# Performance work log

Hardware: AMD Instinct MI355X
Metric: run time of the kernel (lower is better)

The kernel has to match this reference:

```python
import jax, jax.numpy as jnp
import numpy as np

B, S, HID = 1, 2048, 2048
NUM_HEADS, NUM_KV_HEADS, HEAD_DIM = 16, 4, 128
ROPE_THETA = 10000.0
EPS = 1e-6


def setup_inputs() -> dict:
    key = jax.random.key(0)
    ks = jax.random.split(key, 9)
    s = 0.02
    return {
        "hidden_states": jax.random.normal(ks[0], (B, S, HID), jnp.float32),
        "mu_prev": jax.random.normal(ks[1], (B, S, HID), jnp.float32),
        "wq": jax.random.normal(ks[2], (NUM_HEADS * HEAD_DIM, HID), jnp.float32) * s,
        "wk": jax.random.normal(ks[3], (NUM_KV_HEADS * HEAD_DIM, HID), jnp.float32) * s,
        "wv": jax.random.normal(ks[4], (NUM_KV_HEADS * HEAD_DIM, HID), jnp.float32) * s,
        "wo": jax.random.normal(ks[5], (HID, NUM_HEADS * HEAD_DIM), jnp.float32) * s,
        "wmq": jax.random.normal(ks[6], (NUM_HEADS * HEAD_DIM, HID), jnp.float32) * (s * 0.1),
        "wmk": jax.random.normal(ks[7], (NUM_KV_HEADS * HEAD_DIM, HID), jnp.float32) * (s * 0.1),
        "wmv": jax.random.normal(ks[8], (NUM_KV_HEADS * HEAD_DIM, HID), jnp.float32) * (s * 0.1),
        "q_norm_w": jnp.ones((HEAD_DIM,), jnp.float32),
        "k_norm_w": jnp.ones((HEAD_DIM,), jnp.float32),
    }


def _rmsnorm(x, w):
    var = jnp.mean(jnp.square(x), axis=-1, keepdims=True)
    return x * jax.lax.rsqrt(var + EPS) * w


def _rope_cos_sin(seq_len, dtype):
    inv_freq = 1.0 / (ROPE_THETA ** (jnp.arange(0, HEAD_DIM, 2, dtype=jnp.float32) / HEAD_DIM))
    freqs = jnp.arange(seq_len, dtype=jnp.float32)[:, None] * inv_freq[None, :]  # [S, D/2]
    emb = jnp.concatenate([freqs, freqs], axis=-1)  # [S, D]
    return jnp.cos(emb).astype(dtype), jnp.sin(emb).astype(dtype)


def _rotate_half(x):
    x1, x2 = jnp.split(x, 2, axis=-1)
    return jnp.concatenate([-x2, x1], axis=-1)


def reference(hidden_states, mu_prev, wq, wk, wv, wo, wmq, wmk, wmv, q_norm_w, k_norm_w):
    b, s, _ = hidden_states.shape
    # Fused mu-guided QKV projections (cat(x, mu) @ cat(W, Wm)^T == x@W^T + mu@Wm^T)
    q = hidden_states @ wq.T + mu_prev @ wmq.T  # [B,S,H*D]
    k = hidden_states @ wk.T + mu_prev @ wmk.T  # [B,S,KV*D]
    v = hidden_states @ wv.T + mu_prev @ wmv.T
    q = q.reshape(b, s, NUM_HEADS, HEAD_DIM).transpose(0, 2, 1, 3)      # [B,H,S,D]
    k = k.reshape(b, s, NUM_KV_HEADS, HEAD_DIM).transpose(0, 2, 1, 3)   # [B,KV,S,D]
    v = v.reshape(b, s, NUM_KV_HEADS, HEAD_DIM).transpose(0, 2, 1, 3)
    # per-head QK RMSNorm
    q = _rmsnorm(q, q_norm_w)
    k = _rmsnorm(k, k_norm_w)
    # RoPE
    cos, sin = _rope_cos_sin(s, q.dtype)
    q = q * cos + _rotate_half(q) * sin
    k = k * cos + _rotate_half(k) * sin
    # GQA attention without materializing repeated K/V: group query heads
    g = NUM_HEADS // NUM_KV_HEADS
    qg = q.reshape(b, NUM_KV_HEADS, g, s, HEAD_DIM)
    scale = 1.0 / jnp.sqrt(jnp.asarray(HEAD_DIM, q.dtype))
    scores = jnp.einsum('bkgqd,bkld->bkgql', qg, k) * scale  # [B,KV,G,S,S]
    causal = jnp.tril(jnp.ones((s, s), bool))
    scores = jnp.where(causal, scores, jnp.asarray(-jnp.inf, scores.dtype))
    probs = jax.nn.softmax(scores.astype(jnp.float32), axis=-1).astype(q.dtype)
    out = jnp.einsum('bkgql,bkld->bkgqd', probs, v)  # [B,KV,G,S,D]
    out = out.reshape(b, NUM_HEADS, s, HEAD_DIM).transpose(0, 2, 1, 3).reshape(b, s, NUM_HEADS * HEAD_DIM)
    return out @ wo.T
```

## Files before the change

kernel.cpp:

```cpp
#include <hip/hip_runtime.h>
#include <math.h>

#define SEQ 2048
#define HID_DIM 2048
#define NH 16
#define NKV 4
#define HD 128
#define QS 3072

typedef float  f4v  __attribute__((ext_vector_type(4)));
typedef __bf16 bf8v __attribute__((ext_vector_type(8)));
typedef __bf16 bf4v __attribute__((ext_vector_type(4)));
typedef __bf16 bf2v __attribute__((ext_vector_type(2)));

typedef __attribute__((address_space(1))) const void* gvp;
typedef __attribute__((address_space(3))) void*       svp;

__device__ __forceinline__ void gld16(const void* g, void* lds_wave_base) {
    __builtin_amdgcn_global_load_lds((gvp)g, (svp)lds_wave_base, 16, 0, 0);
}

__global__ __launch_bounds__(256)
void cvt_cat2(__bf16* __restrict__ dst, const float* __restrict__ s0,
              const float* __restrict__ s1, int rows, int kq)
{
    int i = blockIdx.x * 256 + threadIdx.x;
    if (i >= rows * kq * 2) return;
    int row = i / (2 * kq), c = i - row * 2 * kq;
    const float* s = (c < kq) ? s0 + ((size_t)row * kq + c) * 4
                              : s1 + ((size_t)row * kq + (c - kq)) * 4;
    float4 v = *reinterpret_cast<const float4*>(s);
    *reinterpret_cast<bf4v*>(dst + ((size_t)row * 2 * kq + c) * 4) =
        bf4v{ (__bf16)v.x, (__bf16)v.y, (__bf16)v.z, (__bf16)v.w };
}

__global__ __launch_bounds__(256)
void cvt(__bf16* __restrict__ dst, const float* __restrict__ src, int n4)
{
    int i = blockIdx.x * 256 + threadIdx.x;
    if (i >= n4) return;
    float4 v = *reinterpret_cast<const float4*>(src + (size_t)i * 4);
    *reinterpret_cast<bf4v*>(dst + (size_t)i * 4) =
        bf4v{ (__bf16)v.x, (__bf16)v.y, (__bf16)v.z, (__bf16)v.w };
}

__global__ __launch_bounds__(256)
void gemm_nt(const __bf16* __restrict__ A, const __bf16* __restrict__ B,
             float* __restrict__ C, int M, int N, int K)
{
    __shared__ __bf16 As[128 * 32];
    __shared__ __bf16 Bs[64 * 32];
    const int tid = threadIdx.x, lane = tid & 63, w = tid >> 6;
    const int wm = w >> 1, wn = w & 1;
    const int mm = lane & 15, quad = lane >> 4;
    const int m0 = blockIdx.y * 128, n0 = blockIdx.x * 64;
    const int r0 = lane >> 2, c0 = (lane & 3) * 8;

    f4v acc[4][2] = {};

    for (int k0 = 0; k0 < K; k0 += 32) {
#pragma unroll
        for (int j = 0; j < 2; ++j) {
            int chunk = w * 2 + j;
            gld16(&A[(size_t)(m0 + chunk * 16 + r0) * K + k0 + c0], (char*)As + chunk * 1024);
        }
        gld16(&B[(size_t)(n0 + w * 16 + r0) * K + k0 + c0], (char*)Bs + w * 1024);
        __syncthreads();
        bf8v af[4], bfv[2];
#pragma unroll
        for (int t = 0; t < 4; ++t)
            af[t] = *reinterpret_cast<const bf8v*>(&As[(wm * 64 + t * 16 + mm) * 32 + quad * 8]);
#pragma unroll
        for (int n = 0; n < 2; ++n)
            bfv[n] = *reinterpret_cast<const bf8v*>(&Bs[(wn * 32 + n * 16 + mm) * 32 + quad * 8]);
#pragma unroll
        for (int mt = 0; mt < 4; ++mt)
#pragma unroll
            for (int nt = 0; nt < 2; ++nt)
                acc[mt][nt] = __builtin_amdgcn_mfma_f32_16x16x32_bf16(af[mt], bfv[nt], acc[mt][nt], 0, 0, 0);
        __syncthreads();
    }
#pragma unroll
    for (int mt = 0; mt < 4; ++mt)
#pragma unroll
        for (int nt = 0; nt < 2; ++nt)
#pragma unroll
            for (int r = 0; r < 4; ++r)
                C[(size_t)(m0 + wm * 64 + mt * 16 + quad * 4 + r) * N
                  + n0 + wn * 32 + nt * 16 + mm] = acc[mt][nt][r];
}

__global__ __launch_bounds__(64)
void norm_rope(float* __restrict__ qkv, const float* __restrict__ qw,
               const float* __restrict__ kw)
{
    const int s = blockIdx.x, hh = blockIdx.y, l = threadIdx.x;
    float* p; const float* wn; float scale;
    if (hh < NH) { p = qkv + (size_t)s * QS + hh * HD;               wn = qw; scale = 0.08838834764831845f; }
    else         { p = qkv + (size_t)s * QS + 2048 + (hh - NH) * HD; wn = kw; scale = 1.0f; }
    float x0 = p[l], x1 = p[l + 64];
    float ss = x0 * x0 + x1 * x1;
#pragma unroll
    for (int off = 32; off; off >>= 1) ss += __shfl_xor(ss, off);
    float inv = rsqrtf(ss * (1.0f / 128.0f) + 1e-6f);
    x0 *= inv * wn[l];
    x1 *= inv * wn[l + 64];
    float invf = exp2f(-(float)l * (13.287712379549449f / 64.0f));
    float ang  = (float)s * invf;
    float c, sn;
    sincosf(ang, &sn, &c);
    p[l]      = (x0 * c - x1 * sn) * scale;
    p[l + 64] = (x1 * c + x0 * sn) * scale;
}

__global__ __launch_bounds__(256)
void pack_k(const float* __restrict__ qkv, __bf16* __restrict__ Kt)
{
    const int kt = blockIdx.x, kh = blockIdx.y, t = threadIdx.x;
    char* tile = (char*)Kt + ((size_t)(kh * 32 + kt)) * 16384;
    const float* src = qkv + 2048 + kh * HD;
#pragma unroll
    for (int i = 0; i < 4; ++i) {
        int cid = t * 4 + i;
        int key = cid >> 4, pc = cid & 15;
        int c = pc ^ (key & 15);
        const float* s = src + (size_t)(kt * 64 + key) * QS + c * 8;
        float4 a = *reinterpret_cast<const float4*>(s);
        float4 b = *reinterpret_cast<const float4*>(s + 4);
        *reinterpret_cast<bf8v*>(tile + cid * 16) =
            bf8v{ (__bf16)a.x, (__bf16)a.y, (__bf16)a.z, (__bf16)a.w,
                  (__bf16)b.x, (__bf16)b.y, (__bf16)b.z, (__bf16)b.w };
    }
}

__global__ __launch_bounds__(256)
void pack_v(const float* __restrict__ qkv, __bf16* __restrict__ Vt)
{
    const int kt = blockIdx.x, kh = blockIdx.y, t = threadIdx.x;
    char* tile = (char*)Vt + ((size_t)(kh * 32 + kt)) * 16384;
    const float* src = qkv + 2560 + kh * HD;
#pragma unroll
    for (int i = 0; i < 4; ++i) {
        int cid = t * 4 + i;
        int d = cid >> 3, kcp = cid & 7;
        int kc = kcp ^ (d & 7);
        const float* s = src + (size_t)(kt * 64 + kc * 8) * QS + d;
        __bf16 tmp[8];
#pragma unroll
        for (int j = 0; j < 8; ++j) tmp[j] = (__bf16)s[(size_t)j * QS];
        *reinterpret_cast<bf8v*>(tile + cid * 16) = *reinterpret_cast<bf8v*>(tmp);
    }
}

__global__ __launch_bounds__(256)
void attn_split(const float* __restrict__ qkv,
                const __bf16* __restrict__ Kt, const __bf16* __restrict__ Vt,
                __bf16* __restrict__ Op, float* __restrict__ Lp)
{
    __shared__ char Ks[16384];
    __shared__ char Vs[16384];
    __shared__ char Ps[4][2048];

    const int c = blockIdx.x, qt = 31 - blockIdx.y, h = blockIdx.z;
    if (c * 8 > qt) return;
    const int kend = min(qt, c * 8 + 7);
    const int tid = threadIdx.x, lane = tid & 63, w = tid >> 6;
    const int mm = lane & 15, quad = lane >> 4;
    const int kh = h >> 2;

    bf8v aq[4];
    const float* qbase = qkv + (size_t)(qt * 64 + w * 16 + mm) * QS + h * HD;
#pragma unroll
    for (int ks = 0; ks < 4; ++ks) {
        float4 f0 = *reinterpret_cast<const float4*>(qbase + ks * 32 + quad * 8);
        float4 f1 = *reinterpret_cast<const float4*>(qbase + ks * 32 + quad * 8 + 4);
        aq[ks] = bf8v{ (__bf16)f0.x, (__bf16)f0.y, (__bf16)f0.z, (__bf16)f0.w,
                       (__bf16)f1.x, (__bf16)f1.y, (__bf16)f1.z, (__bf16)f1.w };
    }

    float lp[4] = {};
    f4v oacc[8] = {};

    for (int kt = c * 8; kt <= kend; ++kt) {
        __syncthreads();
        const char* ktile = (const char*)Kt + ((size_t)(kh * 32 + kt)) * 16384;
        const char* vtile = (const char*)Vt + ((size_t)(kh * 32 + kt)) * 16384;
#pragma unroll
        for (int j = 0; j < 4; ++j) {
            int chunk = w * 4 + j;
            gld16(ktile + chunk * 1024 + lane * 16, Ks + chunk * 1024);
            gld16(vtile + chunk * 1024 + lane * 16, Vs + chunk * 1024);
        }
        __syncthreads();

        f4v s[4] = {};
#pragma unroll
        for (int ks = 0; ks < 4; ++ks)
#pragma unroll
            for (int c16 = 0; c16 < 4; ++c16) {
                bf8v b = *reinterpret_cast<const bf8v*>(
                    Ks + (c16 * 16 + mm) * 256 + (((ks * 4 + quad) ^ mm) << 4));
                s[c16] = __builtin_amdgcn_mfma_f32_16x16x32_bf16(aq[ks], b, s[c16], 0, 0, 0);
            }
        if (kt == qt) {
#pragma unroll
            for (int c16 = 0; c16 < 4; ++c16)
#pragma unroll
                for (int r = 0; r < 4; ++r)
                    if (c16 * 16 + mm > w * 16 + quad * 4 + r)
                        s[c16][r] = -__builtin_inff();
        }
        float pr[4][4];
#pragma unroll
        for (int c16 = 0; c16 < 4; ++c16)
#pragma unroll
            for (int r = 0; r < 4; ++r) {
                pr[c16][r] = __expf(s[c16][r]);
                lp[r] += pr[c16][r];
            }
#pragma unroll
        for (int c16 = 0; c16 < 4; ++c16)
#pragma unroll
            for (int r = 0; r < 4; ++r) {
                float mine  = pr[c16][r];
                float other = __shfl_xor(mine, 1);
                if ((mm & 1) == 0) {
                    int roww = quad * 4 + r;
                    int cc   = c16 * 2 + (mm >> 3);
                    *reinterpret_cast<bf2v*>(
                        &Ps[w][roww * 128 + ((cc ^ (roww & 7)) << 4) + (mm & 7) * 2]) =
                        bf2v{ (__bf16)mine, (__bf16)other };
                }
            }
        bf8v pa[2];
#pragma unroll
        for (int kb = 0; kb < 2; ++kb)
            pa[kb] = *reinterpret_cast<const bf8v*>(
                &Ps[w][mm * 128 + (((kb * 4 + quad) ^ (mm & 7)) << 4)]);
#pragma unroll
        for (int nb = 0; nb < 8; ++nb) {
            int d = nb * 16 + mm;
#pragma unroll
            for (int kb = 0; kb < 2; ++kb) {
                bf8v bv = *reinterpret_cast<const bf8v*>(
                    Vs + d * 128 + (((kb * 4 + quad) ^ (d & 7)) << 4));
                oacc[nb] = __builtin_amdgcn_mfma_f32_16x16x32_bf16(pa[kb], bv, oacc[nb], 0, 0, 0);
            }
        }
    }
#pragma unroll
    for (int off = 1; off < 16; off <<= 1)
#pragma unroll
        for (int r = 0; r < 4; ++r) lp[r] += __shfl_xor(lp[r], off);
#pragma unroll
    for (int r = 0; r < 4; ++r) {
        int row = qt * 64 + w * 16 + quad * 4 + r;
        size_t obase = ((size_t)(c * 16 + h) * SEQ + row) * HD;
#pragma unroll
        for (int nb = 0; nb < 8; ++nb)
            Op[obase + nb * 16 + mm] = (__bf16)oacc[nb][r];
        if (mm == 0)
            Lp[(size_t)(c * 16 + h) * SEQ + row] = lp[r];
    }
}

__global__ __launch_bounds__(64)
void combine(const __bf16* __restrict__ Op, const float* __restrict__ Lp,
             __bf16* __restrict__ ab)
{
    const int row = blockIdx.x, h = blockIdx.y, l = threadIdx.x;
    const int nch = (row >> 9) + 1;
    float L = 0.f, a0 = 0.f, a1 = 0.f;
    for (int c = 0; c < nch; ++c) {
        L += Lp[(size_t)(c * 16 + h) * SEQ + row];
        bf2v p = *reinterpret_cast<const bf2v*>(
            Op + ((size_t)(c * 16 + h) * SEQ + row) * HD + 2 * l);
        a0 += (float)p[0];
        a1 += (float)p[1];
    }
    float inv = 1.f / L;
    *reinterpret_cast<bf2v*>(ab + (size_t)row * (NH * HD) + h * HD + 2 * l) =
        bf2v{ (__bf16)(a0 * inv), (__bf16)(a1 * inv) };
}

extern "C" void kernel_launch(void* const* d_in, const int* in_sizes, int n_in,
                              void* d_out, int out_size, void* d_ws, size_t ws_size,
                              hipStream_t stream)
{
    const float* hs  = (const float*)d_in[0];
    const float* mu  = (const float*)d_in[1];
    const float* wq  = (const float*)d_in[2];
    const float* wk  = (const float*)d_in[3];
    const float* wv  = (const float*)d_in[4];
    const float* wo  = (const float*)d_in[5];
    const float* wmq = (const float*)d_in[6];
    const float* wmk = (const float*)d_in[7];
    const float* wmv = (const float*)d_in[8];
    const float* qw  = (const float*)d_in[9];
    const float* kw  = (const float*)d_in[10];
    float* out = (float*)d_out;

    char* ws = (char*)d_ws;
    __bf16* Wcat = (__bf16*)(ws + 0);
    __bf16* Acat = (__bf16*)(ws + 25165824);
    __bf16* Wo   = (__bf16*)(ws + 41943040);
    float*  qkv  = (float*) (ws + 50331648);
    __bf16* ab   = (__bf16*)(ws + 75497472);
    __bf16* Ktl  = (__bf16*)(ws + 0);
    __bf16* Vtl  = (__bf16*)(ws + 2097152);
    __bf16* Opart= (__bf16*)(ws + 4194304);
    float*  Lpart= (float*) (ws + 37748736);

    cvt_cat2<<<dim3((2048 * 1024 + 255) / 256), 256, 0, stream>>>(Acat, hs, mu, 2048, 512);
    cvt_cat2<<<dim3((2048 * 1024 + 255) / 256), 256, 0, stream>>>(Wcat, wq, wmq, 2048, 512);
    cvt_cat2<<<dim3((512 * 1024 + 255) / 256), 256, 0, stream>>>(Wcat + (size_t)2048 * 4096, wk, wmk, 512, 512);
    cvt_cat2<<<dim3((512 * 1024 + 255) / 256), 256, 0, stream>>>(Wcat + (size_t)2560 * 4096, wv, wmv, 512, 512);
    cvt<<<dim3((1024 * 1024 + 255) / 256), 256, 0, stream>>>(Wo, wo, 1024 * 1024);

    gemm_nt<<<dim3(QS / 64, SEQ / 128), 256, 0, stream>>>(Acat, Wcat, qkv, SEQ, QS, 2 * HID_DIM);
    norm_rope<<<dim3(SEQ, NH + NKV), dim3(64), 0, stream>>>(qkv, qw, kw);
    pack_k<<<dim3(32, NKV), 256, 0, stream>>>(qkv, Ktl);
    pack_v<<<dim3(32, NKV), 256, 0, stream>>>(qkv, Vtl);
    attn_split<<<dim3(4, 32, NH), 256, 0, stream>>>(qkv, Ktl, Vtl, Opart, Lpart);
    combine<<<dim3(SEQ, NH), 64, 0, stream>>>(Opart, Lpart, ab);
    gemm_nt<<<dim3(HID_DIM / 64, SEQ / 128), 256, 0, stream>>>(ab, Wo, out, SEQ, HID_DIM, NH * HD);
}
```

Baseline: 382.5 us.

## Use 128x128 split-K GEMM tiles with bf16 partials and bf16 QKV buffer

Both projection GEMMs now use 128x128 output tiles, which doubles B-tile reuse per block. They also split K across blockIdx.z: two slices for the QKV projection and four for the output projection. Partial results are stored as bf16. The two QKV partials are summed inside norm_rope (for Q and K) and inside pack_v (for V), and a new add4 kernel reduces the four output partials to fp32. This halves the intermediate QKV memory traffic and removes the fp32-to-bf16 conversion loads in the pack and attention kernels. The cost is more rounding from bf16 partial sums, an extra reduction kernel, and extra partial-buffer traffic for the output GEMM.

```diff
diff --git a/kernel.cpp b/kernel.cpp
--- a/kernel.cpp
+++ b/kernel.cpp
@@ -45,63 +45,83 @@
 }
 
 __global__ __launch_bounds__(256)
-void gemm_nt(const __bf16* __restrict__ A, const __bf16* __restrict__ B,
-             float* __restrict__ C, int M, int N, int K)
+void gemm_nt_sp(const __bf16* __restrict__ A, const __bf16* __restrict__ B,
+                __bf16* __restrict__ P, int M, int N, int K, int KS)
 {
     __shared__ __bf16 As[128 * 32];
-    __shared__ __bf16 Bs[64 * 32];
+    __shared__ __bf16 Bs[128 * 32];
     const int tid = threadIdx.x, lane = tid & 63, w = tid >> 6;
     const int wm = w >> 1, wn = w & 1;
     const int mm = lane & 15, quad = lane >> 4;
-    const int m0 = blockIdx.y * 128, n0 = blockIdx.x * 64;
+    const int m0 = blockIdx.y * 128, n0 = blockIdx.x * 128;
+    const int kz0 = blockIdx.z * KS;
     const int r0 = lane >> 2, c0 = (lane & 3) * 8;
 
-    f4v acc[4][2] = {};
-
-    for (int k0 = 0; k0 < K; k0 += 32) {
+    f4v acc[4][4] = {};
+
+    for (int k0 = kz0; k0 < kz0 + KS; k0 += 32) {
 #pragma unroll
         for (int j = 0; j < 2; ++j) {
             int chunk = w * 2 + j;
-            gld16(&A[(size_t)(m0 + chunk * 16 + r0) * K + k0 + c0], (char*)As + chunk * 1024);
-        }
-        gld16(&B[(size_t)(n0 + w * 16 + r0) * K + k0 + c0], (char*)Bs + w * 1024);
+            int row   = chunk * 16 + r0;
+            gld16(&A[(size_t)(m0 + row) * K + k0 + c0], (char*)As + chunk * 1024);
+            gld16(&B[(size_t)(n0 + row) * K + k0 + c0], (char*)Bs + chunk * 1024);
+        }
         __syncthreads();
-        bf8v af[4], bfv[2];
-#pragma unroll
-        for (int t = 0; t < 4; ++t)
-            af[t] = *reinterpret_cast<const bf8v*>(&As[(wm * 64 + t * 16 + mm) * 32 + quad * 8]);
-#pragma unroll
-        for (int n = 0; n < 2; ++n)
-            bfv[n] = *reinterpret_cast<const bf8v*>(&Bs[(wn * 32 + n * 16 + mm) * 32 + quad * 8]);
+        bf8v af[4], bfv[4];
+#pragma unroll
+        for (int t = 0; t < 4; ++t) {
+            af[t]  = *reinterpret_cast<const bf8v*>(&As[(wm * 64 + t * 16 + mm) * 32 + quad * 8]);
+            bfv[t] = *reinterpret_cast<const bf8v*>(&Bs[(wn * 64 + t * 16 + mm) * 32 + quad * 8]);
+        }
 #pragma unroll
         for (int mt = 0; mt < 4; ++mt)
 #pragma unroll
-            for (int nt = 0; nt < 2; ++nt)
+            for (int nt = 0; nt < 4; ++nt)
                 acc[mt][nt] = __builtin_amdgcn_mfma_f32_16x16x32_bf16(af[mt], bfv[nt], acc[mt][nt], 0, 0, 0);
         __syncthreads();
     }
+    __bf16* Pz = P + (size_t)blockIdx.z * M * N;
 #pragma unroll
     for (int mt = 0; mt < 4; ++mt)
 #pragma unroll
-        for (int nt = 0; nt < 2; ++nt)
+        for (int nt = 0; nt < 4; ++nt)
 #pragma unroll
             for (int r = 0; r < 4; ++r)
-                C[(size_t)(m0 + wm * 64 + mt * 16 + quad * 4 + r) * N
-                  + n0 + wn * 32 + nt * 16 + mm] = acc[mt][nt][r];
+                Pz[(size_t)(m0 + wm * 64 + mt * 16 + quad * 4 + r) * N
+                   + n0 + wn * 64 + nt * 16 + mm] = (__bf16)acc[mt][nt][r];
+}
+
+__global__ __launch_bounds__(256)
+void add4(const __bf16* __restrict__ P, float* __restrict__ out, int n4)
+{
+    int i = blockIdx.x * 256 + threadIdx.x;
+    if (i >= n4) return;
+    float4 s = {0.f, 0.f, 0.f, 0.f};
+#pragma unroll
+    for (int z = 0; z < 4; ++z) {
+        bf4v v = *reinterpret_cast<const bf4v*>(P + (size_t)z * n4 * 4 + (size_t)i * 4);
+        s.x += (float)v[0]; s.y += (float)v[1]; s.z += (float)v[2]; s.w += (float)v[3];
+    }
+    *reinterpret_cast<float4*>(out + (size_t)i * 4) = s;
 }
 
 __global__ __launch_bounds__(64)
-void norm_rope(float* __restrict__ qkv, const float* __restrict__ qw,
-               const float* __restrict__ kw)
+void norm_rope(__bf16* __restrict__ qkv ,
+               const __bf16* __restrict__ p1,
+               const float* __restrict__ qw, const float* __restrict__ kw)
 {
     const int s = blockIdx.x, hh = blockIdx.y, l = threadIdx.x;
-    float* p; const float* wn; float scale;
-    if (hh < NH) { p = qkv + (size_t)s * QS + hh * HD;               wn = qw; scale = 0.08838834764831845f; }
-    else         { p = qkv + (size_t)s * QS + 2048 + (hh - NH) * HD; wn = kw; scale = 1.0f; }
-    float x0 = p[l], x1 = p[l + 64];
+    const float* wn; float scale; int off;
+    if (hh < NH) { off = hh * HD;               wn = qw; scale = 0.08838834764831845f; }
+    else         { off = 2048 + (hh - NH) * HD; wn = kw; scale = 1.0f; }
+    __bf16* p = qkv + (size_t)s * QS + off;
+    const __bf16* q1 = p1 + (size_t)s * QS + off;
+    float x0 = (float)p[l]      + (float)q1[l];
+    float x1 = (float)p[l + 64] + (float)q1[l + 64];
     float ss = x0 * x0 + x1 * x1;
 #pragma unroll
-    for (int off = 32; off; off >>= 1) ss += __shfl_xor(ss, off);
+    for (int o = 32; o; o >>= 1) ss += __shfl_xor(ss, o);
     float inv = rsqrtf(ss * (1.0f / 128.0f) + 1e-6f);
     x0 *= inv * wn[l];
     x1 *= inv * wn[l + 64];
@@ -109,51 +129,51 @@
     float ang  = (float)s * invf;
     float c, sn;
     sincosf(ang, &sn, &c);
-    p[l]      = (x0 * c - x1 * sn) * scale;
-    p[l + 64] = (x1 * c + x0 * sn) * scale;
-}
-
-__global__ __launch_bounds__(256)
-void pack_k(const float* __restrict__ qkv, __bf16* __restrict__ Kt)
+    p[l]      = (__bf16)((x0 * c - x1 * sn) * scale);
+    p[l + 64] = (__bf16)((x1 * c + x0 * sn) * scale);
+}
+
+__global__ __launch_bounds__(256)
+void pack_k(const __bf16* __restrict__ qkv, __bf16* __restrict__ Kt)
 {
     const int kt = blockIdx.x, kh = blockIdx.y, t = threadIdx.x;
     char* tile = (char*)Kt + ((size_t)(kh * 32 + kt)) * 16384;
-    const float* src = qkv + 2048 + kh * HD;
+    const __bf16* src = qkv + 2048 + kh * HD;
 #pragma unroll
     for (int i = 0; i < 4; ++i) {
         int cid = t * 4 + i;
         int key = cid >> 4, pc = cid & 15;
         int c = pc ^ (key & 15);
-        const float* s = src + (size_t)(kt * 64 + key) * QS + c * 8;
-        float4 a = *reinterpret_cast<const float4*>(s);
-        float4 b = *reinterpret_cast<const float4*>(s + 4);
-        *reinterpret_cast<bf8v*>(tile + cid * 16) =
-            bf8v{ (__bf16)a.x, (__bf16)a.y, (__bf16)a.z, (__bf16)a.w,
-                  (__bf16)b.x, (__bf16)b.y, (__bf16)b.z, (__bf16)b.w };
-    }
-}
-
-__global__ __launch_bounds__(256)
-void pack_v(const float* __restrict__ qkv, __bf16* __restrict__ Vt)
+        bf8v v = *reinterpret_cast<const bf8v*>(src + (size_t)(kt * 64 + key) * QS + c * 8);
+        *reinterpret_cast<bf8v*>(tile + cid * 16) = v;
+    }
+}
+
+__global__ __launch_bounds__(256)
+void pack_v(const __bf16* __restrict__ qkv0, const __bf16* __restrict__ qkv1,
+            __bf16* __restrict__ Vt)
 {
     const int kt = blockIdx.x, kh = blockIdx.y, t = threadIdx.x;
     char* tile = (char*)Vt + ((size_t)(kh * 32 + kt)) * 16384;
-    const float* src = qkv + 2560 + kh * HD;
+    const __bf16* s0 = qkv0 + 2560 + kh * HD;
+    const __bf16* s1 = qkv1 + 2560 + kh * HD;
 #pragma unroll
     for (int i = 0; i < 4; ++i) {
         int cid = t * 4 + i;
         int d = cid >> 3, kcp = cid & 7;
         int kc = kcp ^ (d & 7);
-        const float* s = src + (size_t)(kt * 64 + kc * 8) * QS + d;
+        size_t base = (size_t)(kt * 64 + kc * 8) * QS + d;
         __bf16 tmp[8];
 #pragma unroll
-        for (int j = 0; j < 8; ++j) tmp[j] = (__bf16)s[(size_t)j * QS];
+        for (int j = 0; j < 8; ++j)
+            tmp[j] = (__bf16)((float)s0[base + (size_t)j * QS] +
+                              (float)s1[base + (size_t)j * QS]);
         *reinterpret_cast<bf8v*>(tile + cid * 16) = *reinterpret_cast<bf8v*>(tmp);
     }
 }
 
 __global__ __launch_bounds__(256)
-void attn_split(const float* __restrict__ qkv,
+void attn_split(const __bf16* __restrict__ qkv,
                 const __bf16* __restrict__ Kt, const __bf16* __restrict__ Vt,
                 __bf16* __restrict__ Op, float* __restrict__ Lp)
 {
@@ -169,14 +189,10 @@
     const int kh = h >> 2;
 
     bf8v aq[4];
-    const float* qbase = qkv + (size_t)(qt * 64 + w * 16 + mm) * QS + h * HD;
-#pragma unroll
-    for (int ks = 0; ks < 4; ++ks) {
-        float4 f0 = *reinterpret_cast<const float4*>(qbase + ks * 32 + quad * 8);
-        float4 f1 = *reinterpret_cast<const float4*>(qbase + ks * 32 + quad * 8 + 4);
-        aq[ks] = bf8v{ (__bf16)f0.x, (__bf16)f0.y, (__bf16)f0.z, (__bf16)f0.w,
-                       (__bf16)f1.x, (__bf16)f1.y, (__bf16)f1.z, (__bf16)f1.w };
-    }
+    const __bf16* qbase = qkv + (size_t)(qt * 64 + w * 16 + mm) * QS + h * HD;
+#pragma unroll
+    for (int ks = 0; ks < 4; ++ks)
+        aq[ks] = *reinterpret_cast<const bf8v*>(qbase + ks * 32 + quad * 8);
 
     float lp[4] = {};
     f4v oacc[8] = {};
@@ -304,12 +320,13 @@
     __bf16* Wcat = (__bf16*)(ws + 0);
     __bf16* Acat = (__bf16*)(ws + 25165824);
     __bf16* Wo   = (__bf16*)(ws + 41943040);
-    float*  qkv  = (float*) (ws + 50331648);
+    __bf16* qkvp = (__bf16*)(ws + 50331648);
     __bf16* ab   = (__bf16*)(ws + 75497472);
     __bf16* Ktl  = (__bf16*)(ws + 0);
     __bf16* Vtl  = (__bf16*)(ws + 2097152);
     __bf16* Opart= (__bf16*)(ws + 4194304);
     float*  Lpart= (float*) (ws + 37748736);
+    __bf16* outp = (__bf16*)(ws + 0);
 
     cvt_cat2<<<dim3((2048 * 1024 + 255) / 256), 256, 0, stream>>>(Acat, hs, mu, 2048, 512);
     cvt_cat2<<<dim3((2048 * 1024 + 255) / 256), 256, 0, stream>>>(Wcat, wq, wmq, 2048, 512);
@@ -317,11 +334,12 @@
     cvt_cat2<<<dim3((512 * 1024 + 255) / 256), 256, 0, stream>>>(Wcat + (size_t)2560 * 4096, wv, wmv, 512, 512);
     cvt<<<dim3((1024 * 1024 + 255) / 256), 256, 0, stream>>>(Wo, wo, 1024 * 1024);
 
-    gemm_nt<<<dim3(QS / 64, SEQ / 128), 256, 0, stream>>>(Acat, Wcat, qkv, SEQ, QS, 2 * HID_DIM);
-    norm_rope<<<dim3(SEQ, NH + NKV), dim3(64), 0, stream>>>(qkv, qw, kw);
-    pack_k<<<dim3(32, NKV), 256, 0, stream>>>(qkv, Ktl);
-    pack_v<<<dim3(32, NKV), 256, 0, stream>>>(qkv, Vtl);
-    attn_split<<<dim3(4, 32, NH), 256, 0, stream>>>(qkv, Ktl, Vtl, Opart, Lpart);
+    gemm_nt_sp<<<dim3(QS / 128, SEQ / 128, 2), 256, 0, stream>>>(Acat, Wcat, qkvp, SEQ, QS, 2 * HID_DIM, HID_DIM);
+    norm_rope<<<dim3(SEQ, NH + NKV), dim3(64), 0, stream>>>(qkvp, qkvp + (size_t)SEQ * QS, qw, kw);
+    pack_k<<<dim3(32, NKV), 256, 0, stream>>>(qkvp, Ktl);
+    pack_v<<<dim3(32, NKV), 256, 0, stream>>>(qkvp, qkvp + (size_t)SEQ * QS, Vtl);
+    attn_split<<<dim3(4, 32, NH), 256, 0, stream>>>(qkvp, Ktl, Vtl, Opart, Lpart);
     combine<<<dim3(SEQ, NH), 64, 0, stream>>>(Opart, Lpart, ab);
-    gemm_nt<<<dim3(HID_DIM / 64, SEQ / 128), 256, 0, stream>>>(ab, Wo, out, SEQ, HID_DIM, NH * HD);
-}
+    gemm_nt_sp<<<dim3(HID_DIM / 128, SEQ / 128, 4), 256, 0, stream>>>(ab, Wo, outp, SEQ, HID_DIM, NH * HD, 512);
+    add4<<<dim3((1024 * 1024 + 255) / 256), 256, 0, stream>>>(outp, out, 1024 * 1024);
+}
```

After: 367.4 us. 3.9% less time.
